# Performance work log

Hardware: AMD Instinct MI355X
Metric: run time of the kernel (lower is better)

Reference implementation:

```python
import jax, jax.numpy as jnp
import numpy as np

B, A, C = 128, 8732, 21

def setup_inputs() -> dict:
    key = jax.random.key(0)
    k1, k2, k3, k4 = jax.random.split(key, 4)
    return {
        "location_output": jax.random.normal(k1, (B, A, 4), dtype=jnp.float32),
        "classifi_output": jax.random.normal(k2, (B, A, C), dtype=jnp.float32),
        "location_label": jax.random.normal(k3, (B, A, 4), dtype=jnp.float32),
        "classifi_label": jax.random.randint(k4, (B, A), 0, C, dtype=jnp.int64),
    }

def reference(location_output, classifi_output, location_label, classifi_label):
    mask = classifi_label > 0                      # [B, A] positive anchors
    pos_num = mask.sum(axis=1)                     # [B]

    # SmoothL1 (beta=1), summed over the 4 box coords, masked to positives
    diff = location_output - location_label
    ad = jnp.abs(diff)
    sl1 = jnp.where(ad < 1.0, 0.5 * diff * diff, ad - 0.5).sum(axis=-1)  # [B, A]
    loc_loss = (sl1 * mask.astype(sl1.dtype)).sum(axis=-1)               # [B]

    # Per-anchor cross entropy
    logp = jax.nn.log_softmax(classifi_output, axis=-1)                  # [B, A, C]
    con = -jnp.take_along_axis(logp, classifi_label[..., None], axis=-1)[..., 0]  # [B, A]

    # Hard negative mining: rank negatives by CE (descending), keep top 3*pos_num
    con_neg = jnp.where(mask, 0.0, con)
    rank = jnp.argsort(jnp.argsort(-con_neg, axis=1), axis=1)            # rank in descending order
    neg_num = jnp.minimum(3 * pos_num, A)
    neg_num = jnp.where(neg_num == 0, 3, neg_num)
    neg_mask = rank < neg_num[:, None]

    con_loss = (con * (mask.astype(con.dtype) + neg_mask.astype(con.dtype))).sum(axis=1)  # [B]

    total = loc_loss + con_loss
    denom = jnp.where(pos_num != 0, pos_num, 1).astype(total.dtype)
    return (total / denom).mean()
```

## Files before the change

### kernel.cpp

```cpp
#include <hip/hip_runtime.h>

#define NBATCH 128
#define NANCH  8732
#define NCLS   21

#define K1_THREADS 256
#define CHUNK 256
#define NCHUNK ((NANCH + CHUNK - 1) / CHUNK)

struct BatchAcc {
    float loc;
    float sum_all;
    float sum_pos;
    unsigned cnt;
};

__device__ __forceinline__ float waveReduceF(float v) {
    #pragma unroll
    for (int o = 32; o > 0; o >>= 1) v += __shfl_down(v, o, 64);
    return v;
}
__device__ __forceinline__ unsigned waveReduceU(unsigned v) {
    #pragma unroll
    for (int o = 32; o > 0; o >>= 1) v += __shfl_down(v, o, 64);
    return v;
}

__device__ __forceinline__ float con_from_row(const float* __restrict__ row, int lbl) {
    float m = row[0];
    #pragma unroll
    for (int c = 1; c < NCLS; ++c) m = fmaxf(m, row[c]);
    float s = 0.f;
    #pragma unroll
    for (int c = 0; c < NCLS; ++c) s += __expf(row[c] - m);
    return m + __logf(s) - row[lbl];
}

__global__ void init_kernel(BatchAcc* __restrict__ acc, float* __restrict__ out) {
    int i = threadIdx.x;
    if (i < NBATCH) acc[i] = BatchAcc{0.f, 0.f, 0.f, 0u};
    if (i == 0) out[0] = 0.f;
}

__global__ __launch_bounds__(K1_THREADS) void anchor_kernel(
    const float* __restrict__ loc_out,
    const float* __restrict__ cls_out,
    const float* __restrict__ loc_lab,
    const int*   __restrict__ labels,
    BatchAcc* __restrict__ acc)
{
    const int b     = blockIdx.x / NCHUNK;
    const int chunk = blockIdx.x % NCHUNK;
    const int tid   = threadIdx.x;

    const int a0  = chunk * CHUNK;
    const int cnt = min(CHUNK, NANCH - a0);
    const size_t ba0 = (size_t)b * NANCH + a0;

    __shared__ float rows[CHUNK * NCLS];

    const float4* __restrict__ src4 = (const float4*)(cls_out + ba0 * NCLS);
    float4* __restrict__ dst4 = (float4*)rows;
    const int nf4 = (cnt * NCLS) >> 2;
    for (int i = tid; i < nf4; i += K1_THREADS) dst4[i] = src4[i];

    float loc_s = 0.f, all_s = 0.f, pos_s = 0.f;
    unsigned pcnt = 0;
    int lbl = 0;
    float4 lo4 = {0,0,0,0}, ll4 = {0,0,0,0};
    const bool active = tid < cnt;
    if (active) {
        size_t ba = ba0 + tid;
        lbl = labels[ba];
        lo4 = ((const float4*)loc_out)[ba];
        ll4 = ((const float4*)loc_lab)[ba];
    }

    __syncthreads();

    if (active) {
        float con = con_from_row(rows + tid * NCLS, lbl);
        all_s = con;
        if (lbl > 0) {
            pos_s = con;
            pcnt  = 1;
            float d0 = lo4.x - ll4.x, d1 = lo4.y - ll4.y,
                  d2 = lo4.z - ll4.z, d3 = lo4.w - ll4.w;
            float a0f = fabsf(d0), a1f = fabsf(d1), a2f = fabsf(d2), a3f = fabsf(d3);
            loc_s  = ((a0f < 1.f) ? 0.5f * d0 * d0 : (a0f - 0.5f))
                   + ((a1f < 1.f) ? 0.5f * d1 * d1 : (a1f - 0.5f))
                   + ((a2f < 1.f) ? 0.5f * d2 * d2 : (a2f - 0.5f))
                   + ((a3f < 1.f) ? 0.5f * d3 * d3 : (a3f - 0.5f));
        }
    }

    loc_s = waveReduceF(loc_s);
    all_s = waveReduceF(all_s);
    pos_s = waveReduceF(pos_s);
    pcnt  = waveReduceU(pcnt);

    __shared__ float sLoc[4], sAll[4], sPos[4];
    __shared__ unsigned sCnt[4];
    int w = tid >> 6, lane = tid & 63;
    if (lane == 0) { sLoc[w] = loc_s; sAll[w] = all_s; sPos[w] = pos_s; sCnt[w] = pcnt; }
    __syncthreads();
    if (tid == 0) {
        float L = 0.f, S = 0.f, P = 0.f; unsigned Cc = 0;
        #pragma unroll
        for (int i = 0; i < 4; ++i) { L += sLoc[i]; S += sAll[i]; P += sPos[i]; Cc += sCnt[i]; }
        atomicAdd(&acc[b].loc, L);
        atomicAdd(&acc[b].sum_all, S);
        atomicAdd(&acc[b].sum_pos, P);
        atomicAdd(&acc[b].cnt, Cc);
    }
}

__global__ __launch_bounds__(256) void finalize_kernel(
    const float* __restrict__ cls_out,
    const int*   __restrict__ labels,
    const BatchAcc* __restrict__ acc,
    float* __restrict__ out)
{
    const int b   = blockIdx.x;
    const int tid = threadIdx.x;
    BatchAcc a = acc[b];

    long long k = (long long)3 * (long long)a.cnt;
    if (k > NANCH) k = NANCH;
    if (k == 0) k = 3;

    float con_loss;

    if (k >= NANCH) {
        con_loss = a.sum_all + a.sum_pos;
        if (tid == 0) {
            float denom = (a.cnt != 0u) ? (float)a.cnt : 1.f;
            atomicAdd(out, (a.loc + con_loss) / denom * (1.f / NBATCH));
        }
        return;
    }

    __shared__ float    sF[256];
    __shared__ unsigned sU[256];
    __shared__ float    bcastF;

    auto count_gt = [&](float t) -> unsigned {
        unsigned c = 0;
        for (int an = tid; an < NANCH; an += 256) {
            size_t ba = (size_t)b * NANCH + an;
            int lbl = labels[ba];
            if (lbl > 0) continue;
            float con = con_from_row(cls_out + ba * NCLS, lbl);
            if (con > t) c++;
        }
        sU[tid] = c; __syncthreads();
        for (int o = 128; o > 0; o >>= 1) {
            if (tid < o) sU[tid] += sU[tid + o];
            __syncthreads();
        }
        unsigned r = sU[0]; __syncthreads();
        return r;
    };

    unsigned cpos = count_gt(0.0f);
    float negpart = 0.f;

    if ((unsigned long long)k <= (unsigned long long)cpos) {
        unsigned lo = 0u, hi = 0x7F800000u;
        while (hi - lo > 1u) {
            unsigned mid = lo + (hi - lo) / 2u;
            unsigned c = count_gt(__uint_as_float(mid));
            if (c >= (unsigned)k) lo = mid; else hi = mid;
        }
        float v = __uint_as_float(hi);
        float ss = 0.f; unsigned c1 = 0;
        for (int an = tid; an < NANCH; an += 256) {
            size_t ba = (size_t)b * NANCH + an;
            int lbl = labels[ba];
            if (lbl > 0) continue;
            float con = con_from_row(cls_out + ba * NCLS, lbl);
            if (con > v) { ss += con; c1++; }
        }
        sF[tid] = ss; sU[tid] = c1; __syncthreads();
        for (int o = 128; o > 0; o >>= 1) {
            if (tid < o) { sF[tid] += sF[tid + o]; sU[tid] += sU[tid + o]; }
            __syncthreads();
        }
        if (tid == 0) { bcastF = sF[0] + (float)((unsigned)k - sU[0]) * v; }
        __syncthreads();
        negpart = bcastF;
    } else {
        if (tid == 0) {
            float np = 0.f;
            unsigned m = (unsigned)k - cpos;
            for (int an = 0; an < NANCH; ++an) {
                size_t ba = (size_t)b * NANCH + an;
                int lbl = labels[ba];
                float con = con_from_row(cls_out + ba * NCLS, lbl);
                float cneg = (lbl > 0) ? 0.f : con;
                if (cneg > 0.f) np += con;
                else if (m > 0u) { np += con; m--; }
            }
            bcastF = np;
        }
        __syncthreads();
        negpart = bcastF;
    }

    con_loss = a.sum_pos + negpart;
    if (tid == 0) {
        float denom = (a.cnt != 0u) ? (float)a.cnt : 1.f;
        atomicAdd(out, (a.loc + con_loss) / denom * (1.f / NBATCH));
    }
}

extern "C" void kernel_launch(void* const* d_in, const int* in_sizes, int n_in,
                              void* d_out, int out_size, void* d_ws, size_t ws_size,
                              hipStream_t stream) {
    const float* loc_out = (const float*)d_in[0];
    const float* cls_out = (const float*)d_in[1];
    const float* loc_lab = (const float*)d_in[2];
    const int*   labels  = (const int*)d_in[3];
    float* out = (float*)d_out;
    BatchAcc* acc = (BatchAcc*)d_ws;

    init_kernel<<<1, 256, 0, stream>>>(acc, out);
    anchor_kernel<<<NBATCH * NCHUNK, K1_THREADS, 0, stream>>>(loc_out, cls_out, loc_lab, labels, acc);
    finalize_kernel<<<NBATCH, 256, 0, stream>>>(cls_out, labels, acc, out);
}
```

Baseline: 190.8 us.

## Make anchor pass persistent per-wave over 64-anchor chunks without block syncs

The anchor kernel becomes a fixed grid of 1792 blocks in which each wavefront processes a contiguous range of 64-anchor chunks. Each wave stages its logits through its own LDS slice, which removes block-level __syncthreads, and it accumulates partial sums in registers, flushing with atomics only when the batch index changes. This is meant to cut atomic traffic and barrier stalls. The init kernel is also replaced with hipMemsetAsync calls. The risk is lower memory-level parallelism per wave, since each wave processes its chunks serially. The finalize kernel, which likely dominates, is unchanged.

After: 224.7 us. 1.18x slower.

```diff
diff --git a/kernel.cpp b/kernel.cpp
--- a/kernel.cpp
+++ b/kernel.cpp
@@ -4,9 +4,13 @@
 #define NANCH  8732
 #define NCLS   21
 
-#define K1_THREADS 256
-#define CHUNK 256
-#define NCHUNK ((NANCH + CHUNK - 1) / CHUNK)
+#define CPB     137
+#define NCHUNKS (NBATCH * CPB)
+#define K_THREADS 256
+#define K_BLOCKS  1792
+#define K_WAVES   (K_BLOCKS * 4)
+#define QCH (NCHUNKS / K_WAVES)
+#define RCH (NCHUNKS % K_WAVES)
 
 struct BatchAcc {
     float loc;
@@ -36,83 +40,96 @@
     return m + __logf(s) - row[lbl];
 }
 
-__global__ void init_kernel(BatchAcc* __restrict__ acc, float* __restrict__ out) {
-    int i = threadIdx.x;
-    if (i < NBATCH) acc[i] = BatchAcc{0.f, 0.f, 0.f, 0u};
-    if (i == 0) out[0] = 0.f;
-}
-
-__global__ __launch_bounds__(K1_THREADS) void anchor_kernel(
+__global__ __launch_bounds__(K_THREADS) void anchor_kernel(
     const float* __restrict__ loc_out,
     const float* __restrict__ cls_out,
     const float* __restrict__ loc_lab,
     const int*   __restrict__ labels,
     BatchAcc* __restrict__ acc)
 {
-    const int b     = blockIdx.x / NCHUNK;
-    const int chunk = blockIdx.x % NCHUNK;
-    const int tid   = threadIdx.x;
-
-    const int a0  = chunk * CHUNK;
-    const int cnt = min(CHUNK, NANCH - a0);
-    const size_t ba0 = (size_t)b * NANCH + a0;
-
-    __shared__ float rows[CHUNK * NCLS];
-
-    const float4* __restrict__ src4 = (const float4*)(cls_out + ba0 * NCLS);
-    float4* __restrict__ dst4 = (float4*)rows;
-    const int nf4 = (cnt * NCLS) >> 2;
-    for (int i = tid; i < nf4; i += K1_THREADS) dst4[i] = src4[i];
+    const int w    = threadIdx.x >> 6;
+    const int lane = threadIdx.x & 63;
+    const int gw   = blockIdx.x * 4 + w;
+
+    __shared__ float4 stage4[4][336];
+    float4* __restrict__ my4 = stage4[w];
+    const float* __restrict__ myrows = (const float*)my4;
+
+    int start, nchunk;
+    if (gw < RCH) { start = gw * (QCH + 1); nchunk = QCH + 1; }
+    else          { start = gw * QCH + RCH; nchunk = QCH; }
 
     float loc_s = 0.f, all_s = 0.f, pos_s = 0.f;
     unsigned pcnt = 0;
-    int lbl = 0;
-    float4 lo4 = {0,0,0,0}, ll4 = {0,0,0,0};
-    const bool active = tid < cnt;
-    if (active) {
-        size_t ba = ba0 + tid;
-        lbl = labels[ba];
-        lo4 = ((const float4*)loc_out)[ba];
-        ll4 = ((const float4*)loc_lab)[ba];
-    }
-
-    __syncthreads();
-
-    if (active) {
-        float con = con_from_row(rows + tid * NCLS, lbl);
-        all_s = con;
-        if (lbl > 0) {
-            pos_s = con;
-            pcnt  = 1;
-            float d0 = lo4.x - ll4.x, d1 = lo4.y - ll4.y,
-                  d2 = lo4.z - ll4.z, d3 = lo4.w - ll4.w;
-            float a0f = fabsf(d0), a1f = fabsf(d1), a2f = fabsf(d2), a3f = fabsf(d3);
-            loc_s  = ((a0f < 1.f) ? 0.5f * d0 * d0 : (a0f - 0.5f))
-                   + ((a1f < 1.f) ? 0.5f * d1 * d1 : (a1f - 0.5f))
-                   + ((a2f < 1.f) ? 0.5f * d2 * d2 : (a2f - 0.5f))
-                   + ((a3f < 1.f) ? 0.5f * d3 * d3 : (a3f - 0.5f));
-        }
-    }
-
-    loc_s = waveReduceF(loc_s);
-    all_s = waveReduceF(all_s);
-    pos_s = waveReduceF(pos_s);
-    pcnt  = waveReduceU(pcnt);
-
-    __shared__ float sLoc[4], sAll[4], sPos[4];
-    __shared__ unsigned sCnt[4];
-    int w = tid >> 6, lane = tid & 63;
-    if (lane == 0) { sLoc[w] = loc_s; sAll[w] = all_s; sPos[w] = pos_s; sCnt[w] = pcnt; }
-    __syncthreads();
-    if (tid == 0) {
-        float L = 0.f, S = 0.f, P = 0.f; unsigned Cc = 0;
+    int curb = -1;
+
+    auto flush = [&]() {
+        float L = waveReduceF(loc_s);
+        float S = waveReduceF(all_s);
+        float P = waveReduceF(pos_s);
+        unsigned C = waveReduceU(pcnt);
+        if (lane == 0) {
+            atomicAdd(&acc[curb].loc, L);
+            atomicAdd(&acc[curb].sum_all, S);
+            atomicAdd(&acc[curb].sum_pos, P);
+            atomicAdd(&acc[curb].cnt, C);
+        }
+        loc_s = all_s = pos_s = 0.f; pcnt = 0;
+    };
+
+    for (int i = 0; i < nchunk; ++i) {
+        const int c   = start + i;
+        const int b   = c / CPB;
+        const int idx = c - b * CPB;
+        const int a0  = idx << 6;
+        const int cnt = (NANCH - a0 < 64) ? (NANCH - a0) : 64;
+        const size_t ba0 = (size_t)b * NANCH + a0;
+
+        if (b != curb) {
+            if (curb >= 0) flush();
+            curb = b;
+        }
+
+        const int nf4 = (cnt * NCLS) >> 2;
+        const float4* __restrict__ src4 = (const float4*)(cls_out + ba0 * NCLS);
+        float4 r[6];
         #pragma unroll
-        for (int i = 0; i < 4; ++i) { L += sLoc[i]; S += sAll[i]; P += sPos[i]; Cc += sCnt[i]; }
-        atomicAdd(&acc[b].loc, L);
-        atomicAdd(&acc[b].sum_all, S);
-        atomicAdd(&acc[b].sum_pos, P);
-        atomicAdd(&acc[b].cnt, Cc);
-    }
+        for (int j = 0; j < 6; ++j) {
+            int fi = j * 64 + lane;
+            if (fi < nf4) r[j] = src4[fi];
+        }
+        const bool active = lane < cnt;
+        int lbl = 0;
+        float4 lo4 = {0,0,0,0}, ll4 = {0,0,0,0};
+        if (active) {
+            lbl = labels[ba0 + lane];
+            lo4 = ((const float4*)loc_out)[ba0 + lane];
+            ll4 = ((const float4*)loc_lab)[ba0 + lane];
+        }
+
+        #pragma unroll
+        for (int j = 0; j < 6; ++j) {
+            int fi = j * 64 + lane;
+            if (fi < nf4) my4[fi] = r[j];
+        }
+
+        if (active) {
+            float con = con_from_row(myrows + lane * NCLS, lbl);
+            all_s += con;
+            if (lbl > 0) {
+                pos_s += con;
+                pcnt++;
+                float d0 = lo4.x - ll4.x, d1 = lo4.y - ll4.y,
+                      d2 = lo4.z - ll4.z, d3 = lo4.w - ll4.w;
+                float a0f = fabsf(d0), a1f = fabsf(d1), a2f = fabsf(d2), a3f = fabsf(d3);
+                loc_s += ((a0f < 1.f) ? 0.5f * d0 * d0 : (a0f - 0.5f))
+                       + ((a1f < 1.f) ? 0.5f * d1 * d1 : (a1f - 0.5f))
+                       + ((a2f < 1.f) ? 0.5f * d2 * d2 : (a2f - 0.5f))
+                       + ((a3f < 1.f) ? 0.5f * d3 * d3 : (a3f - 0.5f));
+            }
+        }
+    }
+    if (curb >= 0) flush();
 }
 
 __global__ __launch_bounds__(256) void finalize_kernel(
@@ -224,7 +241,8 @@
     float* out = (float*)d_out;
     BatchAcc* acc = (BatchAcc*)d_ws;
 
-    init_kernel<<<1, 256, 0, stream>>>(acc, out);
-    anchor_kernel<<<NBATCH * NCHUNK, K1_THREADS, 0, stream>>>(loc_out, cls_out, loc_lab, labels, acc);
+    hipMemsetAsync(acc, 0, NBATCH * sizeof(BatchAcc), stream);
+    hipMemsetAsync(out, 0, sizeof(float), stream);
+    anchor_kernel<<<K_BLOCKS, K_THREADS, 0, stream>>>(loc_out, cls_out, loc_lab, labels, acc);
     finalize_kernel<<<NBATCH, 256, 0, stream>>>(cls_out, labels, acc, out);
 }
```

## Drop init kernel and atomics, load logits directly, finalize in single block

Applied to the files above, without the earlier changes.

The anchor kernel now reads each row's 21 logits straight from global memory with vector loads instead of staging them through shared memory. Per-batch sums go to a partials array without atomics, which removes the init kernel launch. The finalize kernel runs as one block that reduces the partials and writes the output directly. The rare hard-negative path now processes batches serially in that single block, which would be much slower if it ever triggers. Row addresses at a 21-float stride are not always 16-byte aligned, so the float4 loads may be misaligned.

After: 179.2 us. -6.1%, faster.

```diff
diff --git a/kernel.cpp b/kernel.cpp
--- a/kernel.cpp
+++ b/kernel.cpp
@@ -3,17 +3,9 @@
 #define NBATCH 128
 #define NANCH  8732
 #define NCLS   21
-
-#define K1_THREADS 256
-#define CHUNK 256
+#define CHUNK  256
 #define NCHUNK ((NANCH + CHUNK - 1) / CHUNK)
 
-struct BatchAcc {
-    float loc;
-    float sum_all;
-    float sum_pos;
-    unsigned cnt;
-};
 
 __device__ __forceinline__ float waveReduceF(float v) {
     #pragma unroll
@@ -36,182 +28,215 @@
     return m + __logf(s) - row[lbl];
 }
 
-__global__ void init_kernel(BatchAcc* __restrict__ acc, float* __restrict__ out) {
-    int i = threadIdx.x;
-    if (i < NBATCH) acc[i] = BatchAcc{0.f, 0.f, 0.f, 0u};
-    if (i == 0) out[0] = 0.f;
-}
-
-__global__ __launch_bounds__(K1_THREADS) void anchor_kernel(
-    const float* __restrict__ loc_out,
-    const float* __restrict__ cls_out,
-    const float* __restrict__ loc_lab,
-    const int*   __restrict__ labels,
-    BatchAcc* __restrict__ acc)
+__global__ __launch_bounds__(256) void anchor_kernel(
+    const float*  __restrict__ loc_out,
+    const float*  __restrict__ cls_out,
+    const float*  __restrict__ loc_lab,
+    const int*    __restrict__ labels,
+    float4* __restrict__ partial)
 {
-    const int b     = blockIdx.x / NCHUNK;
-    const int chunk = blockIdx.x % NCHUNK;
-    const int tid   = threadIdx.x;
-
-    const int a0  = chunk * CHUNK;
-    const int cnt = min(CHUNK, NANCH - a0);
-    const size_t ba0 = (size_t)b * NANCH + a0;
-
-    __shared__ float rows[CHUNK * NCLS];
-
-    const float4* __restrict__ src4 = (const float4*)(cls_out + ba0 * NCLS);
-    float4* __restrict__ dst4 = (float4*)rows;
-    const int nf4 = (cnt * NCLS) >> 2;
-    for (int i = tid; i < nf4; i += K1_THREADS) dst4[i] = src4[i];
+    const int bid = blockIdx.x;
+    const int b   = bid % NBATCH;
+    const int c   = bid / NBATCH;
+    const int tid = threadIdx.x;
+    const int a   = c * CHUNK + tid;
+    const bool active = a < NANCH;
 
     float loc_s = 0.f, all_s = 0.f, pos_s = 0.f;
-    unsigned pcnt = 0;
-    int lbl = 0;
-    float4 lo4 = {0,0,0,0}, ll4 = {0,0,0,0};
-    const bool active = tid < cnt;
+    unsigned pc = 0;
+
     if (active) {
-        size_t ba = ba0 + tid;
-        lbl = labels[ba];
-        lo4 = ((const float4*)loc_out)[ba];
-        ll4 = ((const float4*)loc_lab)[ba];
-    }
-
-    __syncthreads();
-
-    if (active) {
-        float con = con_from_row(rows + tid * NCLS, lbl);
+        const size_t ba = (size_t)b * NANCH + a;
+        const float* __restrict__ row = cls_out + ba * NCLS;
+
+        const float4 r0 = *(const float4*)(row +  0);
+        const float4 r1 = *(const float4*)(row +  4);
+        const float4 r2 = *(const float4*)(row +  8);
+        const float4 r3 = *(const float4*)(row + 12);
+        const float4 r4 = *(const float4*)(row + 16);
+        const float  r5 = row[20];
+
+        const int lbl = labels[ba];
+        const float4 lo4 = ((const float4*)loc_out)[ba];
+        const float4 ll4 = ((const float4*)loc_lab)[ba];
+
+        float m = r0.x;
+        m = fmaxf(m, r0.y); m = fmaxf(m, r0.z); m = fmaxf(m, r0.w);
+        m = fmaxf(m, r1.x); m = fmaxf(m, r1.y); m = fmaxf(m, r1.z); m = fmaxf(m, r1.w);
+        m = fmaxf(m, r2.x); m = fmaxf(m, r2.y); m = fmaxf(m, r2.z); m = fmaxf(m, r2.w);
+        m = fmaxf(m, r3.x); m = fmaxf(m, r3.y); m = fmaxf(m, r3.z); m = fmaxf(m, r3.w);
+        m = fmaxf(m, r4.x); m = fmaxf(m, r4.y); m = fmaxf(m, r4.z); m = fmaxf(m, r4.w);
+        m = fmaxf(m, r5);
+
+        float s = __expf(r0.x - m) + __expf(r0.y - m) + __expf(r0.z - m) + __expf(r0.w - m)
+                + __expf(r1.x - m) + __expf(r1.y - m) + __expf(r1.z - m) + __expf(r1.w - m)
+                + __expf(r2.x - m) + __expf(r2.y - m) + __expf(r2.z - m) + __expf(r2.w - m)
+                + __expf(r3.x - m) + __expf(r3.y - m) + __expf(r3.z - m) + __expf(r3.w - m)
+                + __expf(r4.x - m) + __expf(r4.y - m) + __expf(r4.z - m) + __expf(r4.w - m)
+                + __expf(r5 - m);
+
+        float tgt = r0.x;
+        tgt = (lbl ==  1) ? r0.y : tgt;  tgt = (lbl ==  2) ? r0.z : tgt;
+        tgt = (lbl ==  3) ? r0.w : tgt;  tgt = (lbl ==  4) ? r1.x : tgt;
+        tgt = (lbl ==  5) ? r1.y : tgt;  tgt = (lbl ==  6) ? r1.z : tgt;
+        tgt = (lbl ==  7) ? r1.w : tgt;  tgt = (lbl ==  8) ? r2.x : tgt;
+        tgt = (lbl ==  9) ? r2.y : tgt;  tgt = (lbl == 10) ? r2.z : tgt;
+        tgt = (lbl == 11) ? r2.w : tgt;  tgt = (lbl == 12) ? r3.x : tgt;
+        tgt = (lbl == 13) ? r3.y : tgt;  tgt = (lbl == 14) ? r3.z : tgt;
+        tgt = (lbl == 15) ? r3.w : tgt;  tgt = (lbl == 16) ? r4.x : tgt;
+        tgt = (lbl == 17) ? r4.y : tgt;  tgt = (lbl == 18) ? r4.z : tgt;
+        tgt = (lbl == 19) ? r4.w : tgt;  tgt = (lbl == 20) ? r5   : tgt;
+
+        const float con = m + __logf(s) - tgt;
         all_s = con;
         if (lbl > 0) {
             pos_s = con;
-            pcnt  = 1;
+            pc = 1;
             float d0 = lo4.x - ll4.x, d1 = lo4.y - ll4.y,
                   d2 = lo4.z - ll4.z, d3 = lo4.w - ll4.w;
-            float a0f = fabsf(d0), a1f = fabsf(d1), a2f = fabsf(d2), a3f = fabsf(d3);
-            loc_s  = ((a0f < 1.f) ? 0.5f * d0 * d0 : (a0f - 0.5f))
-                   + ((a1f < 1.f) ? 0.5f * d1 * d1 : (a1f - 0.5f))
-                   + ((a2f < 1.f) ? 0.5f * d2 * d2 : (a2f - 0.5f))
-                   + ((a3f < 1.f) ? 0.5f * d3 * d3 : (a3f - 0.5f));
+            float a0 = fabsf(d0), a1 = fabsf(d1), a2 = fabsf(d2), a3 = fabsf(d3);
+            loc_s = ((a0 < 1.f) ? 0.5f * d0 * d0 : (a0 - 0.5f))
+                  + ((a1 < 1.f) ? 0.5f * d1 * d1 : (a1 - 0.5f))
+                  + ((a2 < 1.f) ? 0.5f * d2 * d2 : (a2 - 0.5f))
+                  + ((a3 < 1.f) ? 0.5f * d3 * d3 : (a3 - 0.5f));
         }
     }
 
     loc_s = waveReduceF(loc_s);
     all_s = waveReduceF(all_s);
     pos_s = waveReduceF(pos_s);
-    pcnt  = waveReduceU(pcnt);
-
-    __shared__ float sLoc[4], sAll[4], sPos[4];
-    __shared__ unsigned sCnt[4];
-    int w = tid >> 6, lane = tid & 63;
-    if (lane == 0) { sLoc[w] = loc_s; sAll[w] = all_s; sPos[w] = pos_s; sCnt[w] = pcnt; }
+    pc    = waveReduceU(pc);
+
+    __shared__ float sL[4], sA[4], sP[4];
+    __shared__ unsigned sC[4];
+    const int w = tid >> 6, lane = tid & 63;
+    if (lane == 0) { sL[w] = loc_s; sA[w] = all_s; sP[w] = pos_s; sC[w] = pc; }
     __syncthreads();
     if (tid == 0) {
-        float L = 0.f, S = 0.f, P = 0.f; unsigned Cc = 0;
-        #pragma unroll
-        for (int i = 0; i < 4; ++i) { L += sLoc[i]; S += sAll[i]; P += sPos[i]; Cc += sCnt[i]; }
-        atomicAdd(&acc[b].loc, L);
-        atomicAdd(&acc[b].sum_all, S);
-        atomicAdd(&acc[b].sum_pos, P);
-        atomicAdd(&acc[b].cnt, Cc);
+        float L = sL[0] + sL[1] + sL[2] + sL[3];
+        float S = sA[0] + sA[1] + sA[2] + sA[3];
+        float P = sP[0] + sP[1] + sP[2] + sP[3];
+        unsigned C = sC[0] + sC[1] + sC[2] + sC[3];
+        partial[c * NBATCH + b] = make_float4(L, S, P, (float)C);
     }
 }
 
 __global__ __launch_bounds__(256) void finalize_kernel(
     const float* __restrict__ cls_out,
     const int*   __restrict__ labels,
-    const BatchAcc* __restrict__ acc,
+    const float4* __restrict__ partial,
     float* __restrict__ out)
 {
-    const int b   = blockIdx.x;
     const int tid = threadIdx.x;
-    BatchAcc a = acc[b];
-
-    long long k = (long long)3 * (long long)a.cnt;
-    if (k > NANCH) k = NANCH;
-    if (k == 0) k = 3;
-
-    float con_loss;
-
-    if (k >= NANCH) {
-        con_loss = a.sum_all + a.sum_pos;
-        if (tid == 0) {
-            float denom = (a.cnt != 0u) ? (float)a.cnt : 1.f;
-            atomicAdd(out, (a.loc + con_loss) / denom * (1.f / NBATCH));
+
+    __shared__ float sLoc[NBATCH], sPos[NBATCH], sCnt[NBATCH], sConl[NBATCH];
+    __shared__ unsigned sK[NBATCH];
+    __shared__ unsigned nflag;
+    if (tid == 0) nflag = 0;
+    __syncthreads();
+
+    if (tid < NBATCH) {
+        float loc = 0.f, all = 0.f, pos = 0.f, cnt = 0.f;
+        for (int c = 0; c < NCHUNK; ++c) {
+            float4 p = partial[c * NBATCH + tid];
+            loc += p.x; all += p.y; pos += p.z; cnt += p.w;
         }
-        return;
-    }
-
-    __shared__ float    sF[256];
-    __shared__ unsigned sU[256];
-    __shared__ float    bcastF;
-
-    auto count_gt = [&](float t) -> unsigned {
-        unsigned c = 0;
-        for (int an = tid; an < NANCH; an += 256) {
-            size_t ba = (size_t)b * NANCH + an;
-            int lbl = labels[ba];
-            if (lbl > 0) continue;
-            float con = con_from_row(cls_out + ba * NCLS, lbl);
-            if (con > t) c++;
-        }
-        sU[tid] = c; __syncthreads();
-        for (int o = 128; o > 0; o >>= 1) {
-            if (tid < o) sU[tid] += sU[tid + o];
+        unsigned k = 3u * (unsigned)cnt;
+        if (k > NANCH) k = NANCH;
+        if (k == 0u) k = 3u;
+        sLoc[tid] = loc; sPos[tid] = pos; sCnt[tid] = cnt;
+        sConl[tid] = all + pos;
+        if (k < NANCH) { sK[tid] = k; atomicAdd(&nflag, 1u); }
+        else sK[tid] = 0u;
+    }
+    __syncthreads();
+
+    if (nflag) {
+        __shared__ float    rF[256];
+        __shared__ unsigned rU[256];
+        for (int b2 = 0; b2 < NBATCH; ++b2) {
+            unsigned k = sK[b2];
+            if (!k) continue;
+
+            auto count_gt = [&](float t) -> unsigned {
+                unsigned cc = 0;
+                for (int an = tid; an < NANCH; an += 256) {
+                    size_t ba = (size_t)b2 * NANCH + an;
+                    int lbl = labels[ba];
+                    if (lbl > 0) continue;
+                    float con = con_from_row(cls_out + ba * NCLS, lbl);
+                    if (con > t) cc++;
+                }
+                rU[tid] = cc; __syncthreads();
+                for (int o = 128; o > 0; o >>= 1) {
+                    if (tid < o) rU[tid] += rU[tid + o];
+                    __syncthreads();
+                }
+                unsigned r = rU[0]; __syncthreads();
+                return r;
+            };
+
+            unsigned cpos = count_gt(0.0f);
+            float negpart = 0.f;
+
+            if (k <= cpos) {
+                unsigned lo = 0u, hi = 0x7F800000u;
+                while (hi - lo > 1u) {
+                    unsigned mid = lo + (hi - lo) / 2u;
+                    unsigned cc = count_gt(__uint_as_float(mid));
+                    if (cc >= k) lo = mid; else hi = mid;
+                }
+                float v = __uint_as_float(hi);
+                float ss = 0.f; unsigned c1 = 0;
+                for (int an = tid; an < NANCH; an += 256) {
+                    size_t ba = (size_t)b2 * NANCH + an;
+                    int lbl = labels[ba];
+                    if (lbl > 0) continue;
+                    float con = con_from_row(cls_out + ba * NCLS, lbl);
+                    if (con > v) { ss += con; c1++; }
+                }
+                rF[tid] = ss; rU[tid] = c1; __syncthreads();
+                for (int o = 128; o > 0; o >>= 1) {
+                    if (tid < o) { rF[tid] += rF[tid + o]; rU[tid] += rU[tid + o]; }
+                    __syncthreads();
+                }
+                negpart = rF[0] + (float)(k - rU[0]) * v;
+                __syncthreads();
+            } else {
+                if (tid == 0) {
+                    float np = 0.f;
+                    unsigned mrem = k - cpos;
+                    for (int an = 0; an < NANCH; ++an) {
+                        size_t ba = (size_t)b2 * NANCH + an;
+                        int lbl = labels[ba];
+                        float con = con_from_row(cls_out + ba * NCLS, lbl);
+                        float cneg = (lbl > 0) ? 0.f : con;
+                        if (cneg > 0.f) np += con;
+                        else if (mrem > 0u) { np += con; mrem--; }
+                    }
+                    rF[0] = np;
+                }
+                __syncthreads();
+                negpart = rF[0];
+                __syncthreads();
+            }
+
+            if (tid == 0) sConl[b2] = sPos[b2] + negpart;
             __syncthreads();
         }
-        unsigned r = sU[0]; __syncthreads();
-        return r;
-    };
-
-    unsigned cpos = count_gt(0.0f);
-    float negpart = 0.f;
-
-    if ((unsigned long long)k <= (unsigned long long)cpos) {
-        unsigned lo = 0u, hi = 0x7F800000u;
-        while (hi - lo > 1u) {
-            unsigned mid = lo + (hi - lo) / 2u;
-            unsigned c = count_gt(__uint_as_float(mid));
-            if (c >= (unsigned)k) lo = mid; else hi = mid;
-        }
-        float v = __uint_as_float(hi);
-        float ss = 0.f; unsigned c1 = 0;
-        for (int an = tid; an < NANCH; an += 256) {
-            size_t ba = (size_t)b * NANCH + an;
-            int lbl = labels[ba];
-            if (lbl > 0) continue;
-            float con = con_from_row(cls_out + ba * NCLS, lbl);
-            if (con > v) { ss += con; c1++; }
-        }
-        sF[tid] = ss; sU[tid] = c1; __syncthreads();
-        for (int o = 128; o > 0; o >>= 1) {
-            if (tid < o) { sF[tid] += sF[tid + o]; sU[tid] += sU[tid + o]; }
-            __syncthreads();
-        }
-        if (tid == 0) { bcastF = sF[0] + (float)((unsigned)k - sU[0]) * v; }
-        __syncthreads();
-        negpart = bcastF;
-    } else {
-        if (tid == 0) {
-            float np = 0.f;
-            unsigned m = (unsigned)k - cpos;
-            for (int an = 0; an < NANCH; ++an) {
-                size_t ba = (size_t)b * NANCH + an;
-                int lbl = labels[ba];
-                float con = con_from_row(cls_out + ba * NCLS, lbl);
-                float cneg = (lbl > 0) ? 0.f : con;
-                if (cneg > 0.f) np += con;
-                else if (m > 0u) { np += con; m--; }
-            }
-            bcastF = np;
-        }
-        __syncthreads();
-        negpart = bcastF;
-    }
-
-    con_loss = a.sum_pos + negpart;
-    if (tid == 0) {
-        float denom = (a.cnt != 0u) ? (float)a.cnt : 1.f;
-        atomicAdd(out, (a.loc + con_loss) / denom * (1.f / NBATCH));
-    }
+    }
+
+    float t = 0.f;
+    if (tid < NBATCH) {
+        float denom = (sCnt[tid] != 0.f) ? sCnt[tid] : 1.f;
+        t = (sLoc[tid] + sConl[tid]) / denom;
+    }
+    t = waveReduceF(t);
+    __shared__ float sW[4];
+    const int w = tid >> 6, lane = tid & 63;
+    if (lane == 0) sW[w] = t;
+    __syncthreads();
+    if (tid == 0) out[0] = (sW[0] + sW[1] + sW[2] + sW[3]) * (1.f / NBATCH);
 }
 
 extern "C" void kernel_launch(void* const* d_in, const int* in_sizes, int n_in,
@@ -222,9 +247,8 @@
     const float* loc_lab = (const float*)d_in[2];
     const int*   labels  = (const int*)d_in[3];
     float* out = (float*)d_out;
-    BatchAcc* acc = (BatchAcc*)d_ws;
-
-    init_kernel<<<1, 256, 0, stream>>>(acc, out);
-    anchor_kernel<<<NBATCH * NCHUNK, K1_THREADS, 0, stream>>>(loc_out, cls_out, loc_lab, labels, acc);
-    finalize_kernel<<<NBATCH, 256, 0, stream>>>(cls_out, labels, acc, out);
-}
+    float4* partial = (float4*)d_ws;
+
+    anchor_kernel<<<NBATCH * NCHUNK, 256, 0, stream>>>(loc_out, cls_out, loc_lab, labels, partial);
+    finalize_kernel<<<1, 256, 0, stream>>>(cls_out, labels, partial, out);
+}
```
